# Kernel tuning notes

Measured on AMD Instinct MI355X. Metric: run time of the kernel, lower is better.

The kernel has to match this reference:

```python
import jax, jax.numpy as jnp
import numpy as np

H = 2048        # hidden size
NH = 16         # query heads
NKV = 8         # kv heads
HD = 128        # head dim
I = 8192        # intermediate size
EPS = 1e-6
SPLITS = [4194304, 6291456, 8388608, 12582912, 29360128, 46137344]
TOTAL = 62914560


def setup_inputs() -> dict:
    key = jax.random.key(0)
    k1, k2 = jax.random.split(key)
    B, S = 1, 2048
    hidden_states = jax.random.normal(k1, (B, S, H), dtype=jnp.float32)
    flat_weights = jax.random.normal(k2, (TOTAL,), dtype=jnp.float32) * 0.02
    input_ln_w = jnp.ones((H,), dtype=jnp.float32)
    post_ln_w = jnp.ones((H,), dtype=jnp.float32)
    # RoPE tables (Llama theta=10000)
    inv_freq = 1.0 / (10000.0 ** (np.arange(0, HD, 2, dtype=np.float32) / HD))
    ang = np.arange(S, dtype=np.float32)[:, None] * inv_freq[None, :]   # [S, HD/2]
    emb = np.concatenate([ang, ang], axis=-1)                            # [S, HD]
    cos = jnp.asarray(np.cos(emb), dtype=jnp.float32)
    sin = jnp.asarray(np.sin(emb), dtype=jnp.float32)
    return {"hidden_states": hidden_states, "flat_weights": flat_weights,
            "input_ln_w": input_ln_w, "post_ln_w": post_ln_w, "cos": cos, "sin": sin}


def _rms_norm(x, w):
    var = jnp.mean(x * x, axis=-1, keepdims=True)
    return w * (x * jax.lax.rsqrt(var + EPS))


def _rotate_half(x):
    x1, x2 = jnp.split(x, 2, axis=-1)
    return jnp.concatenate([-x2, x1], axis=-1)


def _apply_rope(q, k, cos, sin):
    # q: [B,NH,S,HD], k: [B,NKV,S,HD]; cos/sin: [S,HD]
    c = cos[None, None, :, :]
    s = sin[None, None, :, :]
    return q * c + _rotate_half(q) * s, k * c + _rotate_half(k) * s


def _decoder_layer(hidden_states, flat_weights, input_ln_w, post_ln_w, cos, sin):
    # Simulates dfloat11_decode output: split flat reconstructed weights
    # (split order in source: q, k, v, o, up, gate, down)
    parts = jnp.split(flat_weights, SPLITS)
    q_w = parts[0].reshape(NH * HD, H)
    k_w = parts[1].reshape(NKV * HD, H)
    v_w = parts[2].reshape(NKV * HD, H)
    o_w = parts[3].reshape(H, NH * HD)
    up_w = parts[4].reshape(I, H)
    gate_w = parts[5].reshape(I, H)
    down_w = parts[6].reshape(H, I)

    B, S, _ = hidden_states.shape
    residual = hidden_states
    x = _rms_norm(hidden_states, input_ln_w)

    q = (x @ q_w.T).reshape(B, S, NH, HD).transpose(0, 2, 1, 3)    # [B,NH,S,HD]
    k = (x @ k_w.T).reshape(B, S, NKV, HD).transpose(0, 2, 1, 3)   # [B,NKV,S,HD]
    v = (x @ v_w.T).reshape(B, S, NKV, HD).transpose(0, 2, 1, 3)
    q, k = _apply_rope(q, k, cos, sin)

    # GQA: repeat kv heads
    rep = NH // NKV
    k = jnp.repeat(k, rep, axis=1)   # [B,NH,S,HD]
    v = jnp.repeat(v, rep, axis=1)

    scores = jnp.einsum("bhqd,bhkd->bhqk", q, k) / jnp.sqrt(jnp.float32(HD))
    causal = jnp.tril(jnp.ones((S, S), dtype=bool))
    scores = jnp.where(causal[None, None], scores, jnp.finfo(scores.dtype).min)
    probs = jax.nn.softmax(scores, axis=-1)
    attn = jnp.einsum("bhqk,bhkd->bhqd", probs, v)                  # [B,NH,S,HD]
    attn = attn.transpose(0, 2, 1, 3).reshape(B, S, NH * HD)
    hidden = residual + attn @ o_w.T

    residual = hidden
    x = _rms_norm(hidden, post_ln_w)
    mlp = (jax.nn.silu(x @ gate_w.T) * (x @ up_w.T)) @ down_w.T
    return residual + mlp


def reference(hidden_states, flat_weights, input_ln_w, post_ln_w, cos, sin):
    return _decoder_layer(hidden_states, flat_weights, input_ln_w, post_ln_w, cos, sin)
```

## Files before the change

kernel.cpp:

```cpp
#include <hip/hip_runtime.h>
#include <type_traits>
#include <cstdint>
#include <cstddef>

typedef __bf16 bf16x8 __attribute__((ext_vector_type(8)));
typedef float  f32x4  __attribute__((ext_vector_type(4)));
typedef unsigned short u16v4 __attribute__((ext_vector_type(4)));
typedef unsigned short u16v8 __attribute__((ext_vector_type(8)));

#define H    2048
#define NH   16
#define NKV  8
#define HD   128
#define II   8192
#define S    2048

__device__ __forceinline__ unsigned short f2bf(float f) {
    union { float f; unsigned u; } v; v.f = f;
    unsigned r = v.u + 0x7fffu + ((v.u >> 16) & 1u);
    return (unsigned short)(r >> 16);
}
__device__ __forceinline__ float bf2f(unsigned short b) {
    union { unsigned u; float f; } v; v.u = ((unsigned)b) << 16;
    return v.f;
}

__device__ __forceinline__ void async16(const unsigned short* g, const unsigned short* l) {
    __builtin_amdgcn_global_load_lds(
        (const __attribute__((address_space(1))) void*)g,
        (__attribute__((address_space(3))) void*)l, 16, 0, 0);
}

__global__ __launch_bounds__(256) void w2bf(const float* __restrict__ src,
                                            unsigned short* __restrict__ dst)
{
    const size_t i = (size_t)blockIdx.x * 256 + threadIdx.x;
    float4 a = ((const float4*)src)[2 * i];
    float4 b = ((const float4*)src)[2 * i + 1];
    u16v8 o;
    o[0] = f2bf(a.x); o[1] = f2bf(a.y); o[2] = f2bf(a.z); o[3] = f2bf(a.w);
    o[4] = f2bf(b.x); o[5] = f2bf(b.y); o[6] = f2bf(b.z); o[7] = f2bf(b.w);
    ((u16v8*)dst)[i] = o;
}

__global__ __launch_bounds__(256) void rmsnorm_kernel(
    const float* __restrict__ x, const float* __restrict__ w,
    unsigned short* __restrict__ out)
{
    __shared__ float red[4];
    const int row = blockIdx.x;
    const int tid = threadIdx.x;
    const float* xr = x + (size_t)row * H;
    float4 v0 = ((const float4*)xr)[tid];
    float4 v1 = ((const float4*)xr)[256 + tid];
    float s = v0.x*v0.x + v0.y*v0.y + v0.z*v0.z + v0.w*v0.w
            + v1.x*v1.x + v1.y*v1.y + v1.z*v1.z + v1.w*v1.w;
    #pragma unroll
    for (int o = 1; o < 64; o <<= 1) s += __shfl_xor(s, o);
    if ((tid & 63) == 0) red[tid >> 6] = s;
    __syncthreads();
    float tot = red[0] + red[1] + red[2] + red[3];
    float rinv = rsqrtf(tot * (1.0f / (float)H) + 1e-6f);
    float4 w0 = ((const float4*)w)[tid];
    float4 w1 = ((const float4*)w)[256 + tid];
    u16v4 o0, o1;
    o0[0] = f2bf(v0.x * w0.x * rinv); o0[1] = f2bf(v0.y * w0.y * rinv);
    o0[2] = f2bf(v0.z * w0.z * rinv); o0[3] = f2bf(v0.w * w0.w * rinv);
    o1[0] = f2bf(v1.x * w1.x * rinv); o1[1] = f2bf(v1.y * w1.y * rinv);
    o1[2] = f2bf(v1.z * w1.z * rinv); o1[3] = f2bf(v1.w * w1.w * rinv);
    unsigned short* orow = out + (size_t)row * H;
    *(u16v4*)&orow[tid * 4]        = o0;
    *(u16v4*)&orow[1024 + tid * 4] = o1;
}

template<typename OutT, bool ATOMIC>
__global__ __launch_bounds__(256) void gemm_bf16(
    const unsigned short* __restrict__ A, const unsigned short* __restrict__ B,
    OutT* __restrict__ C, int M, int N, int K, int lda, int kslice)
{
    __shared__ unsigned short As[128 * 32];
    __shared__ unsigned short Bs[128 * 32];
    const int tid  = threadIdx.x;
    const int wave = tid >> 6, lane = tid & 63;
    const int quad = lane >> 4, l16 = lane & 15;
    const int m0 = blockIdx.y * 128, n0 = blockIdx.x * 128;
    const int wm = (wave >> 1) * 64, wn = (wave & 1) * 64;
    const int kbeg = blockIdx.z * kslice;

    const int sr = lane >> 2;
    const int sc = (lane & 3) * 8;
    const unsigned short* Ag0 = A + (size_t)(m0 + wave * 16 + sr) * lda + sc + kbeg;
    const unsigned short* Ag1 = Ag0 + (size_t)64 * lda;
    const unsigned short* Bg0 = B + (size_t)(n0 + wave * 16 + sr) * K + sc + kbeg;
    const unsigned short* Bg1 = Bg0 + (size_t)64 * K;
    unsigned short* Al0 = &As[(wave * 16) * 32];
    unsigned short* Al1 = &As[(64 + wave * 16) * 32];
    unsigned short* Bl0 = &Bs[(wave * 16) * 32];
    unsigned short* Bl1 = &Bs[(64 + wave * 16) * 32];

    f32x4 acc[4][4] = {};

    for (int k0 = 0; k0 < kslice; k0 += 32) {
        async16(Ag0 + k0, Al0);
        async16(Ag1 + k0, Al1);
        async16(Bg0 + k0, Bl0);
        async16(Bg1 + k0, Bl1);
        __syncthreads();

        bf16x8 af[4], bfm[4];
        #pragma unroll
        for (int i = 0; i < 4; i++)
            af[i] = *(const bf16x8*)&As[(wm + i * 16 + l16) * 32 + quad * 8];
        #pragma unroll
        for (int i = 0; i < 4; i++)
            bfm[i] = *(const bf16x8*)&Bs[(wn + i * 16 + l16) * 32 + quad * 8];
        #pragma unroll
        for (int mi = 0; mi < 4; mi++)
            #pragma unroll
            for (int ni = 0; ni < 4; ni++)
                acc[mi][ni] = __builtin_amdgcn_mfma_f32_16x16x32_bf16(
                    af[mi], bfm[ni], acc[mi][ni], 0, 0, 0);
        __syncthreads();
    }

    #pragma unroll
    for (int mi = 0; mi < 4; mi++) {
        #pragma unroll
        for (int r = 0; r < 4; r++) {
            const int m = m0 + wm + mi * 16 + quad * 4 + r;
            const size_t rowoff = (size_t)m * N;
            #pragma unroll
            for (int ni = 0; ni < 4; ni++) {
                const int n = n0 + wn + ni * 16 + l16;
                float v = acc[mi][ni][r];
                if constexpr (ATOMIC) {
                    atomicAdd((float*)&C[rowoff + n], v);
                } else if constexpr (std::is_same<OutT, float>::value) {
                    C[rowoff + n] = v;
                } else {
                    C[rowoff + n] = f2bf(v);
                }
            }
        }
    }
}

__global__ __launch_bounds__(256) void rope_prep(
    const unsigned short* __restrict__ qkv, const float* __restrict__ cosp,
    const float* __restrict__ sinp,
    unsigned short* __restrict__ q_r, unsigned short* __restrict__ k_r)
{
    const int s = blockIdx.x;
    const int tid = threadIdx.x;
    const unsigned short* row = qkv + (size_t)s * 4096;
    #pragma unroll
    for (int j = 0; j < 12; j++) {
        int e = j * 256 + tid;
        int head = e >> 7, hd = e & 127;
        float v = bf2f(row[e]);
        float part = (hd < 64) ? -bf2f(row[e + 64]) : bf2f(row[e - 64]);
        float c  = cosp[s * HD + hd];
        float sn = sinp[s * HD + hd];
        unsigned short ob = f2bf(v * c + part * sn);
        if (head < NH) q_r[((size_t)head * S + s) * HD + hd] = ob;
        else           k_r[((size_t)(head - NH) * S + s) * HD + hd] = ob;
    }
}

__global__ __launch_bounds__(256) void v_trans(
    const unsigned short* __restrict__ qkv, unsigned short* __restrict__ v_t)
{
    __shared__ unsigned short t[128][66];
    const int s0 = blockIdx.x * 64;
    const int kv = blockIdx.y;
    const int tid = threadIdx.x;
    const unsigned short* base = qkv + 3072 + kv * HD;
    #pragma unroll
    for (int i = 0; i < 4; i++) {
        int idx = i * 256 + tid;
        int s_l = idx >> 4;
        int hd8 = (idx & 15) * 8;
        u16v8 v = *(const u16v8*)(base + (size_t)(s0 + s_l) * 4096 + hd8);
        #pragma unroll
        for (int j = 0; j < 8; j++) t[hd8 + j][s_l] = v[j];
    }
    __syncthreads();
    #pragma unroll
    for (int i = 0; i < 8; i++) {
        int idx = i * 256 + tid;
        int d  = idx >> 4;
        int rm = idx & 15;
        int hh = rm >> 3;
        int s4 = (rm & 7) * 4;
        u16v4 o;
        o[0] = t[d][hh * 32 + s4];     o[1] = t[d][hh * 32 + s4 + 1];
        o[2] = t[d][hh * 32 + s4 + 2]; o[3] = t[d][hh * 32 + s4 + 3];
        size_t tile = (size_t)kv * (S / 32) + (s0 >> 5) + hh;
        *(u16v4*)&v_t[(tile * 128 + d) * 32 + s4] = o;
    }
}

__global__ __launch_bounds__(256) void attn_kernel(
    const unsigned short* __restrict__ q_r, const unsigned short* __restrict__ k_r,
    const unsigned short* __restrict__ v_t, unsigned short* __restrict__ out)
{
    __shared__ unsigned short Ks[32 * 128];
    __shared__ unsigned short Vs[144 * 32];
    __shared__ unsigned short P[4][16][40];
    const int h = blockIdx.y, kv = h >> 1;
    const int qb0 = blockIdx.x * 64;
    const int tid = threadIdx.x;
    const int wave = tid >> 6, lane = tid & 63, quad = lane >> 4, l16 = lane & 15;
    const int qb = qb0 + wave * 16;
    const unsigned short* Q  = q_r + (size_t)h * S * HD;
    const unsigned short* K  = k_r + (size_t)kv * S * HD;
    const unsigned short* Vh = v_t + (size_t)kv * (S / 32) * (128 * 32);

    {
        int e0 = tid * 2;
        Vs[128 * 32 + e0]     = (e0     < 32) ? (unsigned short)0x3F80 : (unsigned short)0;
        Vs[128 * 32 + e0 + 1] = (e0 + 1 < 32) ? (unsigned short)0x3F80 : (unsigned short)0;
    }

    bf16x8 aq[4];
    #pragma unroll
    for (int t = 0; t < 4; t++)
        aq[t] = *(const bf16x8*)&Q[(size_t)(qb + l16) * HD + t * 32 + quad * 8];

    f32x4 o[9] = {};
    float m_i[4] = { -__builtin_inff(), -__builtin_inff(), -__builtin_inff(), -__builtin_inff() };
    const float SCL = 0.08838834764831845f * 1.4426950408889634f;
    const int nk = (qb0 >> 5) + 2;

    const int kr  = (lane >> 4);
    const int kbl = lane & 15;
    const int vr  = (lane >> 2);
    const int vbl = lane & 3;

    for (int kb = 0; kb < nk; kb++) {
        const int kbase = kb * 32;
        const unsigned short* Ktile = K + (size_t)kbase * HD;
        const unsigned short* Vtile = Vh + (size_t)kb * (128 * 32);
        #pragma unroll
        for (int e = 0; e < 2; e++) {
            int r = wave * 8 + e * 4 + kr;
            async16(Ktile + r * 128 + ((kbl ^ (r & 15)) * 8), &Ks[(wave * 8 + e * 4) * 128]);
        }
        #pragma unroll
        for (int e = 0; e < 2; e++) {
            int d = wave * 32 + e * 16 + vr;
            async16(Vtile + d * 32 + ((vbl ^ (d & 3)) * 8), &Vs[(wave * 32 + e * 16) * 32]);
        }
        __syncthreads();

        if (kbase <= qb + 15) {
            f32x4 s0 = {0.f, 0.f, 0.f, 0.f}, s1 = {0.f, 0.f, 0.f, 0.f};
            #pragma unroll
            for (int t = 0; t < 4; t++) {
                int b = t * 4 + quad;
                bf16x8 b0 = *(const bf16x8*)&Ks[l16 * 128 + ((b ^ l16) * 8)];
                bf16x8 b1 = *(const bf16x8*)&Ks[(16 + l16) * 128 + ((b ^ l16) * 8)];
                s0 = __builtin_amdgcn_mfma_f32_16x16x32_bf16(aq[t], b0, s0, 0, 0, 0);
                s1 = __builtin_amdgcn_mfma_f32_16x16x32_bf16(aq[t], b1, s1, 0, 0, 0);
            }
            float alpha[4];
            #pragma unroll
            for (int r = 0; r < 4; r++) {
                const int q = qb + quad * 4 + r;
                float v0 = (kbase + l16      <= q) ? s0[r] * SCL : -__builtin_inff();
                float v1 = (kbase + 16 + l16 <= q) ? s1[r] * SCL : -__builtin_inff();
                float mx = fmaxf(v0, v1);
                #pragma unroll
                for (int d = 1; d < 16; d <<= 1) mx = fmaxf(mx, __shfl_xor(mx, d));
                float nm = fmaxf(m_i[r], mx);
                alpha[r] = exp2f(m_i[r] - nm);
                m_i[r] = nm;
                s0[r] = exp2f(v0 - nm);
                s1[r] = exp2f(v1 - nm);
            }
            #pragma unroll
            for (int ni = 0; ni < 9; ni++)
                #pragma unroll
                for (int r = 0; r < 4; r++) o[ni][r] *= alpha[r];
            #pragma unroll
            for (int r = 0; r < 4; r++) {
                P[wave][quad * 4 + r][l16]      = f2bf(s0[r]);
                P[wave][quad * 4 + r][16 + l16] = f2bf(s1[r]);
            }
            asm volatile("s_waitcnt lgkmcnt(0)" ::: "memory");
            bf16x8 ap = *(const bf16x8*)&P[wave][l16][quad * 8];
            #pragma unroll
            for (int ni = 0; ni < 9; ni++) {
                int d = ni * 16 + l16;
                bf16x8 bv = *(const bf16x8*)&Vs[d * 32 + ((quad ^ (d & 3)) * 8)];
                o[ni] = __builtin_amdgcn_mfma_f32_16x16x32_bf16(ap, bv, o[ni], 0, 0, 0);
            }
        }
        __syncthreads();
    }
    #pragma unroll
    for (int r = 0; r < 4; r++) {
        float lsum = __shfl(o[8][r], quad * 16);
        const float inv = 1.0f / lsum;
        const int qrow = qb + quad * 4 + r;
        #pragma unroll
        for (int ni = 0; ni < 8; ni++)
            out[(size_t)qrow * (NH * HD) + h * HD + ni * 16 + l16] = f2bf(o[ni][r] * inv);
    }
}

__global__ __launch_bounds__(256) void silu_mul(unsigned short* __restrict__ m1)
{
    const size_t i = (size_t)blockIdx.x * 256 + threadIdx.x;
    const size_t e = i * 8;
    const int s = (int)(e >> 13);
    const int c = (int)(e & 8191);
    unsigned short* rowp = m1 + (size_t)s * (2 * II);
    u16v8 u = *(const u16v8*)&rowp[c];
    u16v8 g = *(const u16v8*)&rowp[II + c];
    u16v8 r;
    #pragma unroll
    for (int j = 0; j < 8; j++) {
        float gf = bf2f(g[j]);
        float uf = bf2f(u[j]);
        float sig = 1.0f / (1.0f + exp2f(-gf * 1.4426950408889634f));
        r[j] = f2bf(gf * sig * uf);
    }
    *(u16v8*)&rowp[c] = r;
}

extern "C" void kernel_launch(void* const* d_in, const int* in_sizes, int n_in,
                              void* d_out, int out_size, void* d_ws, size_t ws_size,
                              hipStream_t stream) {
    const float* hs   = (const float*)d_in[0];
    const float* W    = (const float*)d_in[1];
    const float* ln1  = (const float*)d_in[2];
    const float* ln2  = (const float*)d_in[3];
    const float* cosp = (const float*)d_in[4];
    const float* sinp = (const float*)d_in[5];
    float* out = (float*)d_out;
    char* ws = (char*)d_ws;

    unsigned short* Wbuf   = (unsigned short*)(ws + 0);
    unsigned short* x_norm = (unsigned short*)(ws + (64ull  << 20));
    unsigned short* qkv    = (unsigned short*)(ws + (72ull  << 20));
    unsigned short* q_r    = (unsigned short*)(ws + (88ull  << 20));
    unsigned short* k_r    = (unsigned short*)(ws + (96ull  << 20));
    unsigned short* v_t    = (unsigned short*)(ws + (100ull << 20));
    unsigned short* attn_o = (unsigned short*)(ws + (104ull << 20));
    unsigned short* mlp1   = (unsigned short*)(ws + (72ull  << 20));

    w2bf<<<8388608 / 2048, 256, 0, stream>>>(W, Wbuf);
    rmsnorm_kernel<<<S, 256, 0, stream>>>(hs, ln1, x_norm);
    gemm_bf16<unsigned short, false><<<dim3(4096 / 128, S / 128, 1), 256, 0, stream>>>(
        x_norm, Wbuf, qkv, S, 4096, H, H, H);
    rope_prep<<<S, 256, 0, stream>>>(qkv, cosp, sinp, q_r, k_r);
    v_trans<<<dim3(S / 64, NKV), 256, 0, stream>>>(qkv, v_t);
    attn_kernel<<<dim3(S / 64, NH), 256, 0, stream>>>(q_r, k_r, v_t, attn_o);
    w2bf<<<4194304 / 2048, 256, 0, stream>>>(W + 8388608, Wbuf);
    hipMemcpyAsync(out, hs, (size_t)S * H * sizeof(float), hipMemcpyDeviceToDevice, stream);
    gemm_bf16<float, true><<<dim3(H / 128, S / 128, 2), 256, 0, stream>>>(
        attn_o, Wbuf, out, S, H, H, H, H / 2);
    rmsnorm_kernel<<<S, 256, 0, stream>>>(out, ln2, x_norm);
    w2bf<<<33554432 / 2048, 256, 0, stream>>>(W + 12582912, Wbuf);
    gemm_bf16<unsigned short, false><<<dim3((2 * II) / 128, S / 128, 1), 256, 0, stream>>>(
        x_norm, Wbuf, mlp1, S, 2 * II, H, H, H);
    silu_mul<<<(S * II / 8) / 256, 256, 0, stream>>>(mlp1);
    w2bf<<<16777216 / 2048, 256, 0, stream>>>(W + 46137344, Wbuf);
    gemm_bf16<float, true><<<dim3(H / 128, S / 128, 4), 256, 0, stream>>>(
        mlp1, Wbuf, out, S, H, II, 2 * II, II / 4);
}
```

Measured before the change: 945.9 us.

## Fuse SiLU-gate into MLP up GEMM via interleaved weights and raise split-K

```diff
diff --git a/kernel.cpp b/kernel.cpp
--- a/kernel.cpp
+++ b/kernel.cpp
@@ -41,6 +41,24 @@
     o[0] = f2bf(a.x); o[1] = f2bf(a.y); o[2] = f2bf(a.z); o[3] = f2bf(a.w);
     o[4] = f2bf(b.x); o[5] = f2bf(b.y); o[6] = f2bf(b.z); o[7] = f2bf(b.w);
     ((u16v8*)dst)[i] = o;
+}
+
+__global__ __launch_bounds__(256) void w2bf_mlp(const float* __restrict__ src,
+                                                unsigned short* __restrict__ dst)
+{
+    const int p = blockIdx.x;
+    const int g = p >> 7, r = p & 127;
+    const int half = r >> 6;
+    const int c = (g << 6) + (r & 63);
+    const float* s = src + ((size_t)half * II + c) * H;
+    unsigned short* d = dst + (size_t)p * H;
+    const int t = threadIdx.x;
+    float4 a = ((const float4*)s)[2 * t];
+    float4 b = ((const float4*)s)[2 * t + 1];
+    u16v8 o;
+    o[0] = f2bf(a.x); o[1] = f2bf(a.y); o[2] = f2bf(a.z); o[3] = f2bf(a.w);
+    o[4] = f2bf(b.x); o[5] = f2bf(b.y); o[6] = f2bf(b.z); o[7] = f2bf(b.w);
+    *(u16v8*)&d[t * 8] = o;
 }
 
 __global__ __launch_bounds__(256) void rmsnorm_kernel(
@@ -73,13 +91,14 @@
     *(u16v4*)&orow[1024 + tid * 4] = o1;
 }
 
-template<typename OutT, bool ATOMIC>
+template<typename OutT, bool ATOMIC, bool SILU>
 __global__ __launch_bounds__(256) void gemm_bf16(
     const unsigned short* __restrict__ A, const unsigned short* __restrict__ B,
     OutT* __restrict__ C, int M, int N, int K, int lda, int kslice)
 {
-    __shared__ unsigned short As[128 * 32];
-    __shared__ unsigned short Bs[128 * 32];
+    __shared__ unsigned short SM[8192];
+    unsigned short* As = SM;
+    unsigned short* Bs = SM + 4096;
     const int tid  = threadIdx.x;
     const int wave = tid >> 6, lane = tid & 63;
     const int quad = lane >> 4, l16 = lane & 15;
@@ -93,10 +112,10 @@
     const unsigned short* Ag1 = Ag0 + (size_t)64 * lda;
     const unsigned short* Bg0 = B + (size_t)(n0 + wave * 16 + sr) * K + sc + kbeg;
     const unsigned short* Bg1 = Bg0 + (size_t)64 * K;
-    unsigned short* Al0 = &As[(wave * 16) * 32];
-    unsigned short* Al1 = &As[(64 + wave * 16) * 32];
-    unsigned short* Bl0 = &Bs[(wave * 16) * 32];
-    unsigned short* Bl1 = &Bs[(64 + wave * 16) * 32];
+    const unsigned short* Al0 = &As[(wave * 16) * 32];
+    const unsigned short* Al1 = &As[(64 + wave * 16) * 32];
+    const unsigned short* Bl0 = &Bs[(wave * 16) * 32];
+    const unsigned short* Bl1 = &Bs[(64 + wave * 16) * 32];
 
     f32x4 acc[4][4] = {};
 
@@ -121,6 +140,40 @@
                 acc[mi][ni] = __builtin_amdgcn_mfma_f32_16x16x32_bf16(
                     af[mi], bfm[ni], acc[mi][ni], 0, 0, 0);
         __syncthreads();
+    }
+
+    if constexpr (SILU) {
+        if (wave & 1) {
+            #pragma unroll
+            for (int mi = 0; mi < 4; mi++)
+                #pragma unroll
+                for (int r = 0; r < 4; r++) {
+                    const int lm = wm + mi * 16 + quad * 4 + r;
+                    #pragma unroll
+                    for (int ni = 0; ni < 4; ni++)
+                        SM[lm * 64 + ni * 16 + l16] = f2bf(acc[mi][ni][r]);
+                }
+        }
+        __syncthreads();
+        if (!(wave & 1)) {
+            const int colbase = blockIdx.x * 64;
+            #pragma unroll
+            for (int mi = 0; mi < 4; mi++)
+                #pragma unroll
+                for (int r = 0; r < 4; r++) {
+                    const int lm = wm + mi * 16 + quad * 4 + r;
+                    const size_t rowoff = (size_t)(m0 + lm) * N;
+                    #pragma unroll
+                    for (int ni = 0; ni < 4; ni++) {
+                        const int c = ni * 16 + l16;
+                        float g = bf2f(SM[lm * 64 + c]);
+                        float u = acc[mi][ni][r];
+                        float sig = 1.0f / (1.0f + exp2f(-g * 1.4426950408889634f));
+                        C[rowoff + colbase + c] = f2bf(g * sig * u);
+                    }
+                }
+        }
+        return;
     }
 
     #pragma unroll
@@ -146,19 +199,19 @@
 }
 
 __global__ __launch_bounds__(256) void rope_prep(
-    const unsigned short* __restrict__ qkv, const float* __restrict__ cosp,
+    const float* __restrict__ qkv, const float* __restrict__ cosp,
     const float* __restrict__ sinp,
     unsigned short* __restrict__ q_r, unsigned short* __restrict__ k_r)
 {
     const int s = blockIdx.x;
     const int tid = threadIdx.x;
-    const unsigned short* row = qkv + (size_t)s * 4096;
+    const float* row = qkv + (size_t)s * 4096;
     #pragma unroll
     for (int j = 0; j < 12; j++) {
         int e = j * 256 + tid;
         int head = e >> 7, hd = e & 127;
-        float v = bf2f(row[e]);
-        float part = (hd < 64) ? -bf2f(row[e + 64]) : bf2f(row[e - 64]);
+        float v = row[e];
+        float part = (hd < 64) ? -row[e + 64] : row[e - 64];
         float c  = cosp[s * HD + hd];
         float sn = sinp[s * HD + hd];
         unsigned short ob = f2bf(v * c + part * sn);
@@ -168,21 +221,23 @@
 }
 
 __global__ __launch_bounds__(256) void v_trans(
-    const unsigned short* __restrict__ qkv, unsigned short* __restrict__ v_t)
+    const float* __restrict__ qkv, unsigned short* __restrict__ v_t)
 {
     __shared__ unsigned short t[128][66];
     const int s0 = blockIdx.x * 64;
     const int kv = blockIdx.y;
     const int tid = threadIdx.x;
-    const unsigned short* base = qkv + 3072 + kv * HD;
-    #pragma unroll
-    for (int i = 0; i < 4; i++) {
-        int idx = i * 256 + tid;
-        int s_l = idx >> 4;
-        int hd8 = (idx & 15) * 8;
-        u16v8 v = *(const u16v8*)(base + (size_t)(s0 + s_l) * 4096 + hd8);
-        #pragma unroll
-        for (int j = 0; j < 8; j++) t[hd8 + j][s_l] = v[j];
+    const float* base = qkv + 3072 + kv * HD;
+    #pragma unroll
+    for (int i = 0; i < 8; i++) {
+        int idx4 = i * 256 + tid;
+        int s_l = idx4 >> 5;
+        int hd4 = (idx4 & 31) * 4;
+        float4 v = *(const float4*)(base + (size_t)(s0 + s_l) * 4096 + hd4);
+        t[hd4 + 0][s_l] = f2bf(v.x);
+        t[hd4 + 1][s_l] = f2bf(v.y);
+        t[hd4 + 2][s_l] = f2bf(v.z);
+        t[hd4 + 3][s_l] = f2bf(v.w);
     }
     __syncthreads();
     #pragma unroll
@@ -309,26 +364,6 @@
     }
 }
 
-__global__ __launch_bounds__(256) void silu_mul(unsigned short* __restrict__ m1)
-{
-    const size_t i = (size_t)blockIdx.x * 256 + threadIdx.x;
-    const size_t e = i * 8;
-    const int s = (int)(e >> 13);
-    const int c = (int)(e & 8191);
-    unsigned short* rowp = m1 + (size_t)s * (2 * II);
-    u16v8 u = *(const u16v8*)&rowp[c];
-    u16v8 g = *(const u16v8*)&rowp[II + c];
-    u16v8 r;
-    #pragma unroll
-    for (int j = 0; j < 8; j++) {
-        float gf = bf2f(g[j]);
-        float uf = bf2f(u[j]);
-        float sig = 1.0f / (1.0f + exp2f(-gf * 1.4426950408889634f));
-        r[j] = f2bf(gf * sig * uf);
-    }
-    *(u16v8*)&rowp[c] = r;
-}
-
 extern "C" void kernel_launch(void* const* d_in, const int* in_sizes, int n_in,
                               void* d_out, int out_size, void* d_ws, size_t ws_size,
                               hipStream_t stream) {
@@ -343,30 +378,30 @@
 
     unsigned short* Wbuf   = (unsigned short*)(ws + 0);
     unsigned short* x_norm = (unsigned short*)(ws + (64ull  << 20));
-    unsigned short* qkv    = (unsigned short*)(ws + (72ull  << 20));
-    unsigned short* q_r    = (unsigned short*)(ws + (88ull  << 20));
-    unsigned short* k_r    = (unsigned short*)(ws + (96ull  << 20));
-    unsigned short* v_t    = (unsigned short*)(ws + (100ull << 20));
-    unsigned short* attn_o = (unsigned short*)(ws + (104ull << 20));
-    unsigned short* mlp1   = (unsigned short*)(ws + (72ull  << 20));
+    float*          qkv    = (float*)(ws + (72ull  << 20));
+    unsigned short* act    = (unsigned short*)(ws + (72ull  << 20));
+    unsigned short* q_r    = (unsigned short*)(ws + (104ull << 20));
+    unsigned short* k_r    = (unsigned short*)(ws + (112ull << 20));
+    unsigned short* v_t    = (unsigned short*)(ws + (116ull << 20));
+    unsigned short* attn_o = (unsigned short*)(ws + (120ull << 20));
 
     w2bf<<<8388608 / 2048, 256, 0, stream>>>(W, Wbuf);
     rmsnorm_kernel<<<S, 256, 0, stream>>>(hs, ln1, x_norm);
-    gemm_bf16<unsigned short, false><<<dim3(4096 / 128, S / 128, 1), 256, 0, stream>>>(
-        x_norm, Wbuf, qkv, S, 4096, H, H, H);
+    hipMemsetAsync(qkv, 0, (size_t)S * 4096 * sizeof(float), stream);
+    gemm_bf16<float, true, false><<<dim3(4096 / 128, S / 128, 2), 256, 0, stream>>>(
+        x_norm, Wbuf, qkv, S, 4096, H, H, H / 2);
     rope_prep<<<S, 256, 0, stream>>>(qkv, cosp, sinp, q_r, k_r);
     v_trans<<<dim3(S / 64, NKV), 256, 0, stream>>>(qkv, v_t);
     attn_kernel<<<dim3(S / 64, NH), 256, 0, stream>>>(q_r, k_r, v_t, attn_o);
     w2bf<<<4194304 / 2048, 256, 0, stream>>>(W + 8388608, Wbuf);
     hipMemcpyAsync(out, hs, (size_t)S * H * sizeof(float), hipMemcpyDeviceToDevice, stream);
-    gemm_bf16<float, true><<<dim3(H / 128, S / 128, 2), 256, 0, stream>>>(
-        attn_o, Wbuf, out, S, H, H, H, H / 2);
+    gemm_bf16<float, true, false><<<dim3(H / 128, S / 128, 4), 256, 0, stream>>>(
+        attn_o, Wbuf, out, S, H, H, H, H / 4);
     rmsnorm_kernel<<<S, 256, 0, stream>>>(out, ln2, x_norm);
-    w2bf<<<33554432 / 2048, 256, 0, stream>>>(W + 12582912, Wbuf);
-    gemm_bf16<unsigned short, false><<<dim3((2 * II) / 128, S / 128, 1), 256, 0, stream>>>(
-        x_norm, Wbuf, mlp1, S, 2 * II, H, H, H);
-    silu_mul<<<(S * II / 8) / 256, 256, 0, stream>>>(mlp1);
+    w2bf_mlp<<<2 * II, 256, 0, stream>>>(W + 12582912, Wbuf);
+    gemm_bf16<unsigned short, false, true><<<dim3((2 * II) / 128, S / 128, 1), 256, 0, stream>>>(
+        x_norm, Wbuf, act, S, II, H, H, H);
     w2bf<<<16777216 / 2048, 256, 0, stream>>>(W + 46137344, Wbuf);
-    gemm_bf16<float, true><<<dim3(H / 128, S / 128, 4), 256, 0, stream>>>(
-        mlp1, Wbuf, out, S, H, II, 2 * II, II / 4);
-}
+    gemm_bf16<float, true, false><<<dim3(H / 128, S / 128, 8), 256, 0, stream>>>(
+        act, Wbuf, out, S, H, II, II, II / 8);
+}
```

Measured after the change: 994.8 us. 5.2% more time.
